# Performance work log

Measured on AMD Instinct MI355X. Metric: run time of the kernel, lower is better.

Reference implementation:

```python
import jax, jax.numpy as jnp
import numpy as np

B, LC, LM, D = 128, 512, 512, 512

def setup_inputs() -> dict:
    key = jax.random.key(0)
    k1, k2, k3 = jax.random.split(key, 3)
    context = jax.random.normal(k1, (B, LC, D), dtype=jnp.float32)
    main = jax.random.normal(k2, (B, LM, D), dtype=jnp.float32)
    W = jax.random.normal(k3, (D, 1), dtype=jnp.float32)
    return {"context": context, "main": main, "W": W}

def reference(context, main, W):
    # scores[b,c,m] = <context[b,c,:], main[b,m,:]>
    scores = jnp.einsum('bcd,bmd->bcm', context, main)
    # softmax over last axis (main positions), matching K.softmax default axis=-1
    attn = jax.nn.softmax(scores, axis=-1)           # [B, LC, LM]
    # Keras dot(axes=1): contract context-position axis -> [B, LM, D]
    aligned = jnp.einsum('bcm,bcd->bmd', attn, context)
    diff = main - aligned                            # [B, LM, D]
    # project to scalar per main position, softmax over positions
    w = jax.nn.softmax(jnp.einsum('bmd,d->bm', diff, W[:, 0]), axis=-1)  # [B, LM]
    # weighted sum over main positions -> [B, D]
    out = jnp.einsum('bm,bmd->bd', w, diff)
    return out
```

## Files before the change

### kernel.cpp

```cpp
#include <hip/hip_runtime.h>

#define B_  128
#define LC_ 512
#define LM_ 512
#define D_  512

typedef __attribute__((ext_vector_type(8))) short short8;
typedef __attribute__((ext_vector_type(16))) float f32x16;
typedef unsigned int u32;

__device__ __forceinline__ unsigned short bf16_rn(float x) {
  unsigned u = __float_as_uint(x);
  unsigned r = u + 0x7fffu + ((u >> 16) & 1u);
  return (unsigned short)(r >> 16);
}

__device__ __forceinline__ void gl_lds16(const void* g, void* l) {
  __builtin_amdgcn_global_load_lds((const __attribute__((address_space(1))) u32*)g,
                                   (__attribute__((address_space(3))) u32*)l, 16, 0, 0);
}

__global__ __launch_bounds__(256) void k_cvt_main(
    const float* __restrict__ mn, const float* __restrict__ W,
    short* __restrict__ BtH, short* __restrict__ BtL,
    float* __restrict__ v) {
  __shared__ float sW[512];
  int tid = threadIdx.x;
  sW[tid] = W[tid];
  sW[tid + 256] = W[tid + 256];
  __syncthreads();
  int wave = blockIdx.x * 4 + (tid >> 6);
  int b = wave >> 4, mt = wave & 15;
  int lane = tid & 63, rowl = lane & 31, h = lane >> 5;
  const float* src = mn + ((size_t)b * LM_ + 32 * mt + rowl) * D_ + 8 * h;
  float acc = 0.f;
  for (int ks = 0; ks < 32; ks++) {
    float4 f0 = *(const float4*)(src + 16 * ks);
    float4 f1 = *(const float4*)(src + 16 * ks + 4);
    float xs[8] = {f0.x, f0.y, f0.z, f0.w, f1.x, f1.y, f1.z, f1.w};
    int k = 16 * ks + 8 * h;
    float4 w0 = *(const float4*)&sW[k];
    float4 w1 = *(const float4*)&sW[k + 4];
    float ws[8] = {w0.x, w0.y, w0.z, w0.w, w1.x, w1.y, w1.z, w1.w};
    short8 vh, vl;
    #pragma unroll
    for (int e = 0; e < 8; e++) {
      unsigned short hb = bf16_rn(xs[e]);
      float hf = __uint_as_float((unsigned)hb << 16);
      vh[e] = (short)hb;
      vl[e] = (short)bf16_rn(xs[e] - hf);
      acc = fmaf(xs[e], ws[e], acc);
    }
    size_t off = (((size_t)b * 32 + ks) * 16 + mt) * 512 + (size_t)lane * 8;
    *(short8*)(BtH + off) = vh;
    *(short8*)(BtL + off) = vl;
  }
  acc += __shfl_xor(acc, 32, 64);
  if (h == 0) v[b * LM_ + 32 * mt + rowl] = acc;
}

struct __align__(16) Smem3 {
  short8 Bf[2][2][16][64];
  short8 Af[2][2][4][64];
  float sW[512];
  float red[4][128];
  float cmb[128];
  float uld[128];
  float tpw[2][4][128];
};

__global__ __launch_bounds__(512, 2) void k_scores_mfma3(
    const float* __restrict__ ctx, const short* __restrict__ BtH,
    const short* __restrict__ BtL, const float* __restrict__ W,
    float* __restrict__ P, float* __restrict__ tpart) {
  __shared__ Smem3 sm;
  int p = blockIdx.x;
  int b = (p & 7) | ((p >> 5) << 3);
  int cblk = (p >> 3) & 3;
  int c0 = cblk * 128;
  int tid = threadIdx.x;
  int lane = tid & 63, wv = tid >> 6;
  int rowl = lane & 31, h = lane >> 5;

  f32x16 acc[2][4];
  #pragma unroll
  for (int r = 0; r < 2; r++)
    #pragma unroll
    for (int mtl = 0; mtl < 4; mtl++)
      #pragma unroll
      for (int j = 0; j < 16; j++) acc[r][mtl][j] = 0.f;

  auto stageB = [&](int bf, int ks) {
    #pragma unroll
    for (int rep = 0; rep < 2; rep++) {
      int mt = wv + 8 * rep;
      size_t off = (((size_t)b * 32 + ks) * 16 + mt) * 512 + (size_t)lane * 8;
      gl_lds16(BtH + off, &sm.Bf[bf][0][mt][0]);
      gl_lds16(BtL + off, &sm.Bf[bf][1][mt][0]);
    }
  };
  auto cvtA = [&](int bf, int ks, const float4& g0, const float4& g1, float& au) {
    float xs[8] = {g0.x, g0.y, g0.z, g0.w, g1.x, g1.y, g1.z, g1.w};
    int k = 16 * ks + 8 * h;
    float4 w0 = *(const float4*)&sm.sW[k];
    float4 w1 = *(const float4*)&sm.sW[k + 4];
    float ws[8] = {w0.x, w0.y, w0.z, w0.w, w1.x, w1.y, w1.z, w1.w};
    short8 vh, vl;
    #pragma unroll
    for (int e = 0; e < 8; e++) {
      unsigned short hb = bf16_rn(xs[e]);
      float hf = __uint_as_float((unsigned)hb << 16);
      vh[e] = (short)hb;
      vl[e] = (short)bf16_rn(xs[e] - hf);
      au = fmaf(xs[e], ws[e], au);
    }
    *(short8*)&sm.Af[bf][0][wv][lane] = vh;
    *(short8*)&sm.Af[bf][1][wv][lane] = vl;
  };

  sm.sW[tid] = W[tid];
  float accu = 0.f;
  stageB(0, 0);
  const float* arow = ctx + ((size_t)b * LC_ + c0 + 32 * wv + rowl) * D_ + 8 * h;
  float4 g0, g1;
  if (wv < 4) {
    g0 = *(const float4*)(arow);
    g1 = *(const float4*)(arow + 4);
  }
  __syncthreads();
  if (wv < 4) cvtA(0, 0, g0, g1, accu);
  __syncthreads();

  for (int ks = 0; ks < 32; ks++) {
    int buf = ks & 1;
    if (ks < 31) {
      stageB(buf ^ 1, ks + 1);
      if (wv < 4) {
        const float* ap = arow + 16 * (ks + 1);
        g0 = *(const float4*)ap;
        g1 = *(const float4*)(ap + 4);
      }
    }
    int rt0 = (wv >> 2) * 2;
    short8 ah0 = sm.Af[buf][0][rt0][lane];
    short8 ah1 = sm.Af[buf][0][rt0 + 1][lane];
    short8 al0 = sm.Af[buf][1][rt0][lane];
    short8 al1 = sm.Af[buf][1][rt0 + 1][lane];
    #pragma unroll
    for (int mtl = 0; mtl < 4; mtl++) {
      int mtg = (wv & 3) * 4 + mtl;
      short8 bh = sm.Bf[buf][0][mtg][lane];
      short8 bl = sm.Bf[buf][1][mtg][lane];
      acc[0][mtl] = __builtin_amdgcn_mfma_f32_32x32x16_bf16(ah0, bh, acc[0][mtl], 0, 0, 0);
      acc[0][mtl] = __builtin_amdgcn_mfma_f32_32x32x16_bf16(ah0, bl, acc[0][mtl], 0, 0, 0);
      acc[0][mtl] = __builtin_amdgcn_mfma_f32_32x32x16_bf16(al0, bh, acc[0][mtl], 0, 0, 0);
      acc[1][mtl] = __builtin_amdgcn_mfma_f32_32x32x16_bf16(ah1, bh, acc[1][mtl], 0, 0, 0);
      acc[1][mtl] = __builtin_amdgcn_mfma_f32_32x32x16_bf16(ah1, bl, acc[1][mtl], 0, 0, 0);
      acc[1][mtl] = __builtin_amdgcn_mfma_f32_32x32x16_bf16(al1, bh, acc[1][mtl], 0, 0, 0);
    }
    if (ks < 31 && wv < 4) cvtA(buf ^ 1, ks + 1, g0, g1, accu);
    __syncthreads();
  }

  if (wv < 4) {
    accu += __shfl_xor(accu, 32, 64);
    if (h == 0) sm.uld[32 * wv + rowl] = accu;
  }

  #pragma unroll
  for (int r = 0; r < 2; r++)
    #pragma unroll
    for (int j = 0; j < 16; j++) {
      float mx = fmaxf(fmaxf(acc[r][0][j], acc[r][1][j]),
                       fmaxf(acc[r][2][j], acc[r][3][j]));
      #pragma unroll
      for (int s = 1; s <= 16; s <<= 1) mx = fmaxf(mx, __shfl_xor(mx, s, 64));
      if (rowl == 0)
        sm.red[wv & 3][64 * (wv >> 2) + 32 * r + (j & 3) + 8 * (j >> 2) + 4 * h] = mx;
    }
  __syncthreads();
  if (tid < 128)
    sm.cmb[tid] = fmaxf(fmaxf(sm.red[0][tid], sm.red[1][tid]),
                        fmaxf(sm.red[2][tid], sm.red[3][tid]));
  __syncthreads();
  #pragma unroll
  for (int r = 0; r < 2; r++)
    #pragma unroll
    for (int j = 0; j < 16; j++) {
      int row = 64 * (wv >> 2) + 32 * r + (j & 3) + 8 * (j >> 2) + 4 * h;
      float mx = sm.cmb[row];
      float s = 0.f;
      #pragma unroll
      for (int mtl = 0; mtl < 4; mtl++) {
        float e = __expf(acc[r][mtl][j] - mx);
        acc[r][mtl][j] = e;
        s += e;
      }
      #pragma unroll
      for (int st = 1; st <= 16; st <<= 1) s += __shfl_xor(s, st, 64);
      if (rowl == 0) sm.red[wv & 3][row] = s;
    }
  __syncthreads();
  if (tid < 128)
    sm.cmb[tid] = sm.red[0][tid] + sm.red[1][tid] + sm.red[2][tid] + sm.red[3][tid];
  __syncthreads();

  float* Pb = P + ((size_t)b * LC_ + c0) * LM_;
  float tp[4] = {0.f, 0.f, 0.f, 0.f};
  #pragma unroll
  for (int r = 0; r < 2; r++)
    #pragma unroll
    for (int j = 0; j < 16; j++) {
      int row = 64 * (wv >> 2) + 32 * r + (j & 3) + 8 * (j >> 2) + 4 * h;
      float rinv = 1.f / sm.cmb[row];
      float uu = sm.uld[row];
      #pragma unroll
      for (int mtl = 0; mtl < 4; mtl++) {
        float pv = acc[r][mtl][j] * rinv;
        Pb[(size_t)row * LM_ + 128 * (wv & 3) + 32 * mtl + rowl] = pv;
        tp[mtl] = fmaf(pv, uu, tp[mtl]);
      }
    }
  #pragma unroll
  for (int mtl = 0; mtl < 4; mtl++) tp[mtl] += __shfl_xor(tp[mtl], 32, 64);
  if (h == 0) {
    #pragma unroll
    for (int mtl = 0; mtl < 4; mtl++)
      sm.tpw[wv >> 2][wv & 3][32 * mtl + rowl] = tp[mtl];
  }
  __syncthreads();
  {
    int m = tid;
    tpart[((size_t)b * 4 + cblk) * LM_ + m] =
        sm.tpw[0][m >> 7][m & 127] + sm.tpw[1][m >> 7][m & 127];
  }
}

__global__ __launch_bounds__(256) void k_tw(const float* __restrict__ tpart,
                                            const float* __restrict__ v,
                                            float* __restrict__ w_) {
  int b = blockIdx.x;
  int tid = threadIdx.x;
  int m0 = tid * 2;
  const float* tp = tpart + (size_t)b * 4 * LM_;
  float s0 = 0.f, s1 = 0.f;
  #pragma unroll
  for (int cb = 0; cb < 4; cb++) {
    s0 += tp[cb * LM_ + m0];
    s1 += tp[cb * LM_ + m0 + 1];
  }
  float x0 = v[b * LM_ + m0] - s0;
  float x1 = v[b * LM_ + m0 + 1] - s1;
  float mx = fmaxf(x0, x1);
  #pragma unroll
  for (int s = 32; s >= 1; s >>= 1) mx = fmaxf(mx, __shfl_xor(mx, s, 64));
  __shared__ float redm[4], reds[4];
  int wvv = tid >> 6, ln = tid & 63;
  if (ln == 0) redm[wvv] = mx;
  __syncthreads();
  mx = fmaxf(fmaxf(redm[0], redm[1]), fmaxf(redm[2], redm[3]));
  float e0 = __expf(x0 - mx), e1 = __expf(x1 - mx);
  float sum = e0 + e1;
  #pragma unroll
  for (int s = 32; s >= 1; s >>= 1) sum += __shfl_xor(sum, s, 64);
  if (ln == 0) reds[wvv] = sum;
  __syncthreads();
  sum = reds[0] + reds[1] + reds[2] + reds[3];
  float rinv = 1.0f / sum;
  float2 o; o.x = e0 * rinv; o.y = e1 * rinv;
  *(float2*)&w_[b * LM_ + m0] = o;
}

__global__ __launch_bounds__(256) void k_q(const float* __restrict__ P,
                                           const float* __restrict__ w,
                                           float* __restrict__ q) {
  int b = blockIdx.y;
  int c0 = blockIdx.x * 32;
  int wvv = threadIdx.x >> 6, ln = threadIdx.x & 63;
  __shared__ float sw[LM_];
  *(float2*)&sw[threadIdx.x * 2] = *(const float2*)&w[b * LM_ + threadIdx.x * 2];
  __syncthreads();
  #pragma unroll
  for (int rr = 0; rr < 8; rr++) {
    int c = c0 + wvv * 8 + rr;
    const float4* Pr = (const float4*)(P + ((size_t)b * LC_ + c) * LM_) + ln * 2;
    float4 p0 = Pr[0], p1 = Pr[1];
    const float4* wr = (const float4*)sw + ln * 2;
    float4 w0 = wr[0], w1 = wr[1];
    float acc = p0.x*w0.x + p0.y*w0.y + p0.z*w0.z + p0.w*w0.w
              + p1.x*w1.x + p1.y*w1.y + p1.z*w1.z + p1.w*w1.w;
    #pragma unroll
    for (int s = 32; s >= 1; s >>= 1) acc += __shfl_xor(acc, s, 64);
    if (ln == 0) q[b * LC_ + c] = acc;
  }
}

__global__ __launch_bounds__(256) void k_out(const float* __restrict__ ctx,
                                             const float* __restrict__ mn,
                                             const float* __restrict__ w,
                                             const float* __restrict__ q,
                                             float* __restrict__ out) {
  int b = blockIdx.y;
  int d0 = blockIdx.x * 64;
  int td = threadIdx.x & 63;
  int tg = threadIdx.x >> 6;
  const float* Mb = mn  + (size_t)b * LM_ * D_ + d0;
  const float* Cb = ctx + (size_t)b * LC_ * D_ + d0;
  const float* wb = w + b * LM_;
  const float* qb = q + b * LC_;
  float acc = 0.f;
  #pragma unroll 4
  for (int m = tg; m < LM_; m += 4) acc += wb[m] * Mb[(size_t)m * D_ + td];
  #pragma unroll 4
  for (int c = tg; c < LC_; c += 4) acc -= qb[c] * Cb[(size_t)c * D_ + td];
  __shared__ float red[4][64];
  red[tg][td] = acc;
  __syncthreads();
  if (tg == 0)
    out[b * D_ + d0 + td] = red[0][td] + red[1][td] + red[2][td] + red[3][td];
}

extern "C" void kernel_launch(void* const* d_in, const int* in_sizes, int n_in,
                              void* d_out, int out_size, void* d_ws, size_t ws_size,
                              hipStream_t stream) {
  const float* ctx = (const float*)d_in[0];
  const float* mn  = (const float*)d_in[1];
  const float* W   = (const float*)d_in[2];
  float* out = (float*)d_out;

  char* base = (char*)d_ws;
  size_t nPbytes = (size_t)B_ * LC_ * LM_ * 4;
  size_t planeB  = (size_t)B_ * LM_ * D_ * 2;

  float* P   = (float*)base;
  short* BtH = (short*)(base + nPbytes);
  short* BtL = (short*)(base + nPbytes + planeB);
  char* p2 = base + nPbytes + 2 * planeB;
  float* tpart = (float*)p2;  p2 += (size_t)B_ * 4 * LM_ * 4;
  float* v = (float*)p2;      p2 += (size_t)B_ * LM_ * 4;
  float* w = (float*)p2;      p2 += (size_t)B_ * LM_ * 4;
  float* q = (float*)p2;

  k_cvt_main<<<dim3(512), 256, 0, stream>>>(mn, W, BtH, BtL, v);
  k_scores_mfma3<<<dim3(512), 512, 0, stream>>>(ctx, BtH, BtL, W, P, tpart);
  k_tw<<<dim3(B_), 256, 0, stream>>>(tpart, v, w);
  k_q<<<dim3(LC_ / 32, B_), 256, 0, stream>>>(P, w, q);
  k_out<<<dim3(D_ / 64, B_), 256, 0, stream>>>(ctx, mn, w, q, out);
}
```

Measured before the change: 281.8 us.

## Retile scores kernel to 64-row blocks with per-wave in-register A conversion

The scores kernel moves from 512-thread blocks covering 128 context rows to 256-thread blocks covering 64 rows, launched over twice as many blocks. Each wave now loads and splits its own context rows into bf16 hi/lo in registers, which removes the shared-memory A staging buffer and the extra barrier that went with it. Partial tp sums are written straight to an 8-way tpart array, and k_tw reduces over 8 slices instead of 4. The trade-off is that every wave redundantly converts the same A rows and global B staging doubles per output row, in exchange for less LDS use, fewer barriers and more blocks to spread across the device.

```diff
diff --git a/kernel.cpp b/kernel.cpp
--- a/kernel.cpp
+++ b/kernel.cpp
@@ -19,6 +19,13 @@
   __builtin_amdgcn_global_load_lds((const __attribute__((address_space(1))) u32*)g,
                                    (__attribute__((address_space(3))) u32*)l, 16, 0, 0);
 }
+
+#define CVT1(SRC, WS, AH, AL, IDX, ACCU)                         \
+  { unsigned short hb_ = bf16_rn(SRC);                           \
+    float hf_ = __uint_as_float((u32)hb_ << 16);                 \
+    AH[IDX] = (short)hb_;                                        \
+    AL[IDX] = (short)bf16_rn((SRC) - hf_);                       \
+    ACCU = fmaf((SRC), (WS), ACCU); }
 
 __global__ __launch_bounds__(256) void k_cvt_main(
     const float* __restrict__ mn, const float* __restrict__ W,
@@ -37,20 +44,14 @@
   for (int ks = 0; ks < 32; ks++) {
     float4 f0 = *(const float4*)(src + 16 * ks);
     float4 f1 = *(const float4*)(src + 16 * ks + 4);
-    float xs[8] = {f0.x, f0.y, f0.z, f0.w, f1.x, f1.y, f1.z, f1.w};
     int k = 16 * ks + 8 * h;
     float4 w0 = *(const float4*)&sW[k];
     float4 w1 = *(const float4*)&sW[k + 4];
-    float ws[8] = {w0.x, w0.y, w0.z, w0.w, w1.x, w1.y, w1.z, w1.w};
     short8 vh, vl;
-    #pragma unroll
-    for (int e = 0; e < 8; e++) {
-      unsigned short hb = bf16_rn(xs[e]);
-      float hf = __uint_as_float((unsigned)hb << 16);
-      vh[e] = (short)hb;
-      vl[e] = (short)bf16_rn(xs[e] - hf);
-      acc = fmaf(xs[e], ws[e], acc);
-    }
+    CVT1(f0.x, w0.x, vh, vl, 0, acc); CVT1(f0.y, w0.y, vh, vl, 1, acc);
+    CVT1(f0.z, w0.z, vh, vl, 2, acc); CVT1(f0.w, w0.w, vh, vl, 3, acc);
+    CVT1(f1.x, w1.x, vh, vl, 4, acc); CVT1(f1.y, w1.y, vh, vl, 5, acc);
+    CVT1(f1.z, w1.z, vh, vl, 6, acc); CVT1(f1.w, w1.w, vh, vl, 7, acc);
     size_t off = (((size_t)b * 32 + ks) * 16 + mt) * 512 + (size_t)lane * 8;
     *(short8*)(BtH + off) = vh;
     *(short8*)(BtL + off) = vl;
@@ -59,127 +60,117 @@
   if (h == 0) v[b * LM_ + 32 * mt + rowl] = acc;
 }
 
-struct __align__(16) Smem3 {
+struct __align__(16) Smem4 {
   short8 Bf[2][2][16][64];
-  short8 Af[2][2][4][64];
   float sW[512];
-  float red[4][128];
-  float cmb[128];
-  float uld[128];
-  float tpw[2][4][128];
+  float red[4][64];
+  float cmb[64];
+  float uld[64];
 };
 
-__global__ __launch_bounds__(512, 2) void k_scores_mfma3(
+__global__ __launch_bounds__(256, 2) void k_scores_mfma5(
     const float* __restrict__ ctx, const short* __restrict__ BtH,
     const short* __restrict__ BtL, const float* __restrict__ W,
     float* __restrict__ P, float* __restrict__ tpart) {
-  __shared__ Smem3 sm;
+  __shared__ Smem4 sm;
   int p = blockIdx.x;
-  int b = (p & 7) | ((p >> 5) << 3);
-  int cblk = (p >> 3) & 3;
-  int c0 = cblk * 128;
+  int b = (p & 7) | ((p >> 6) << 3);
+  int cblk = (p >> 3) & 7;
+  int c0 = cblk * 64;
   int tid = threadIdx.x;
   int lane = tid & 63, wv = tid >> 6;
   int rowl = lane & 31, h = lane >> 5;
 
-  f32x16 acc[2][4];
-  #pragma unroll
-  for (int r = 0; r < 2; r++)
-    #pragma unroll
-    for (int mtl = 0; mtl < 4; mtl++)
-      #pragma unroll
-      for (int j = 0; j < 16; j++) acc[r][mtl][j] = 0.f;
+  f32x16 acc0[4], acc1[4];
+  #pragma unroll
+  for (int m = 0; m < 4; m++)
+    #pragma unroll
+    for (int j = 0; j < 16; j++) { acc0[m][j] = 0.f; acc1[m][j] = 0.f; }
 
   auto stageB = [&](int bf, int ks) {
     #pragma unroll
-    for (int rep = 0; rep < 2; rep++) {
-      int mt = wv + 8 * rep;
+    for (int rep = 0; rep < 4; rep++) {
+      int mt = wv + 4 * rep;
       size_t off = (((size_t)b * 32 + ks) * 16 + mt) * 512 + (size_t)lane * 8;
       gl_lds16(BtH + off, &sm.Bf[bf][0][mt][0]);
       gl_lds16(BtL + off, &sm.Bf[bf][1][mt][0]);
     }
   };
-  auto cvtA = [&](int bf, int ks, const float4& g0, const float4& g1, float& au) {
-    float xs[8] = {g0.x, g0.y, g0.z, g0.w, g1.x, g1.y, g1.z, g1.w};
+
+  const float* ar0 = ctx + ((size_t)b * LC_ + c0 +      rowl) * D_ + 8 * h;
+  const float* ar1 = ctx + ((size_t)b * LC_ + c0 + 32 + rowl) * D_ + 8 * h;
+
+  sm.sW[tid] = W[tid];
+  sm.sW[tid + 256] = W[tid + 256];
+  stageB(0, 0);
+  float accu0 = 0.f, accu1 = 0.f;
+  __syncthreads();
+
+  for (int ks = 0; ks < 32; ks++) {
+    int buf = ks & 1;
+    if (ks < 31) stageB(buf ^ 1, ks + 1);
+
     int k = 16 * ks + 8 * h;
     float4 w0 = *(const float4*)&sm.sW[k];
     float4 w1 = *(const float4*)&sm.sW[k + 4];
-    float ws[8] = {w0.x, w0.y, w0.z, w0.w, w1.x, w1.y, w1.z, w1.w};
-    short8 vh, vl;
-    #pragma unroll
-    for (int e = 0; e < 8; e++) {
-      unsigned short hb = bf16_rn(xs[e]);
-      float hf = __uint_as_float((unsigned)hb << 16);
-      vh[e] = (short)hb;
-      vl[e] = (short)bf16_rn(xs[e] - hf);
-      au = fmaf(xs[e], ws[e], au);
-    }
-    *(short8*)&sm.Af[bf][0][wv][lane] = vh;
-    *(short8*)&sm.Af[bf][1][wv][lane] = vl;
-  };
-
-  sm.sW[tid] = W[tid];
-  float accu = 0.f;
-  stageB(0, 0);
-  const float* arow = ctx + ((size_t)b * LC_ + c0 + 32 * wv + rowl) * D_ + 8 * h;
-  float4 g0, g1;
-  if (wv < 4) {
-    g0 = *(const float4*)(arow);
-    g1 = *(const float4*)(arow + 4);
-  }
-  __syncthreads();
-  if (wv < 4) cvtA(0, 0, g0, g1, accu);
-  __syncthreads();
-
-  for (int ks = 0; ks < 32; ks++) {
-    int buf = ks & 1;
-    if (ks < 31) {
-      stageB(buf ^ 1, ks + 1);
-      if (wv < 4) {
-        const float* ap = arow + 16 * (ks + 1);
-        g0 = *(const float4*)ap;
-        g1 = *(const float4*)(ap + 4);
-      }
-    }
-    int rt0 = (wv >> 2) * 2;
-    short8 ah0 = sm.Af[buf][0][rt0][lane];
-    short8 ah1 = sm.Af[buf][0][rt0 + 1][lane];
-    short8 al0 = sm.Af[buf][1][rt0][lane];
-    short8 al1 = sm.Af[buf][1][rt0 + 1][lane];
+    short8 ah0, al0, ah1, al1;
+    {
+      const float* p0 = ar0 + 16 * ks;
+      float4 g0 = *(const float4*)p0;
+      float4 g1 = *(const float4*)(p0 + 4);
+      CVT1(g0.x, w0.x, ah0, al0, 0, accu0); CVT1(g0.y, w0.y, ah0, al0, 1, accu0);
+      CVT1(g0.z, w0.z, ah0, al0, 2, accu0); CVT1(g0.w, w0.w, ah0, al0, 3, accu0);
+      CVT1(g1.x, w1.x, ah0, al0, 4, accu0); CVT1(g1.y, w1.y, ah0, al0, 5, accu0);
+      CVT1(g1.z, w1.z, ah0, al0, 6, accu0); CVT1(g1.w, w1.w, ah0, al0, 7, accu0);
+    }
+    {
+      const float* p1 = ar1 + 16 * ks;
+      float4 g0 = *(const float4*)p1;
+      float4 g1 = *(const float4*)(p1 + 4);
+      CVT1(g0.x, w0.x, ah1, al1, 0, accu1); CVT1(g0.y, w0.y, ah1, al1, 1, accu1);
+      CVT1(g0.z, w0.z, ah1, al1, 2, accu1); CVT1(g0.w, w0.w, ah1, al1, 3, accu1);
+      CVT1(g1.x, w1.x, ah1, al1, 4, accu1); CVT1(g1.y, w1.y, ah1, al1, 5, accu1);
+      CVT1(g1.z, w1.z, ah1, al1, 6, accu1); CVT1(g1.w, w1.w, ah1, al1, 7, accu1);
+    }
+
     #pragma unroll
     for (int mtl = 0; mtl < 4; mtl++) {
-      int mtg = (wv & 3) * 4 + mtl;
-      short8 bh = sm.Bf[buf][0][mtg][lane];
-      short8 bl = sm.Bf[buf][1][mtg][lane];
-      acc[0][mtl] = __builtin_amdgcn_mfma_f32_32x32x16_bf16(ah0, bh, acc[0][mtl], 0, 0, 0);
-      acc[0][mtl] = __builtin_amdgcn_mfma_f32_32x32x16_bf16(ah0, bl, acc[0][mtl], 0, 0, 0);
-      acc[0][mtl] = __builtin_amdgcn_mfma_f32_32x32x16_bf16(al0, bh, acc[0][mtl], 0, 0, 0);
-      acc[1][mtl] = __builtin_amdgcn_mfma_f32_32x32x16_bf16(ah1, bh, acc[1][mtl], 0, 0, 0);
-      acc[1][mtl] = __builtin_amdgcn_mfma_f32_32x32x16_bf16(ah1, bl, acc[1][mtl], 0, 0, 0);
-      acc[1][mtl] = __builtin_amdgcn_mfma_f32_32x32x16_bf16(al1, bh, acc[1][mtl], 0, 0, 0);
-    }
-    if (ks < 31 && wv < 4) cvtA(buf ^ 1, ks + 1, g0, g1, accu);
+      int mt = 4 * wv + mtl;
+      short8 bh = sm.Bf[buf][0][mt][lane];
+      short8 bl = sm.Bf[buf][1][mt][lane];
+      acc0[mtl] = __builtin_amdgcn_mfma_f32_32x32x16_bf16(ah0, bh, acc0[mtl], 0, 0, 0);
+      acc0[mtl] = __builtin_amdgcn_mfma_f32_32x32x16_bf16(ah0, bl, acc0[mtl], 0, 0, 0);
+      acc0[mtl] = __builtin_amdgcn_mfma_f32_32x32x16_bf16(al0, bh, acc0[mtl], 0, 0, 0);
+      acc1[mtl] = __builtin_amdgcn_mfma_f32_32x32x16_bf16(ah1, bh, acc1[mtl], 0, 0, 0);
+      acc1[mtl] = __builtin_amdgcn_mfma_f32_32x32x16_bf16(ah1, bl, acc1[mtl], 0, 0, 0);
+      acc1[mtl] = __builtin_amdgcn_mfma_f32_32x32x16_bf16(al1, bh, acc1[mtl], 0, 0, 0);
+    }
     __syncthreads();
   }
 
-  if (wv < 4) {
-    accu += __shfl_xor(accu, 32, 64);
-    if (h == 0) sm.uld[32 * wv + rowl] = accu;
+  accu0 += __shfl_xor(accu0, 32, 64);
+  accu1 += __shfl_xor(accu1, 32, 64);
+  if (wv == 0 && h == 0) {
+    sm.uld[rowl] = accu0;
+    sm.uld[32 + rowl] = accu1;
   }
 
   #pragma unroll
   for (int r = 0; r < 2; r++)
     #pragma unroll
     for (int j = 0; j < 16; j++) {
-      float mx = fmaxf(fmaxf(acc[r][0][j], acc[r][1][j]),
-                       fmaxf(acc[r][2][j], acc[r][3][j]));
+      float a0 = r ? acc1[0][j] : acc0[0][j];
+      float a1 = r ? acc1[1][j] : acc0[1][j];
+      float a2 = r ? acc1[2][j] : acc0[2][j];
+      float a3 = r ? acc1[3][j] : acc0[3][j];
+      float mx = fmaxf(fmaxf(a0, a1), fmaxf(a2, a3));
       #pragma unroll
       for (int s = 1; s <= 16; s <<= 1) mx = fmaxf(mx, __shfl_xor(mx, s, 64));
       if (rowl == 0)
-        sm.red[wv & 3][64 * (wv >> 2) + 32 * r + (j & 3) + 8 * (j >> 2) + 4 * h] = mx;
-    }
-  __syncthreads();
-  if (tid < 128)
+        sm.red[wv][32 * r + (j & 3) + 8 * (j >> 2) + 4 * h] = mx;
+    }
+  __syncthreads();
+  if (tid < 64)
     sm.cmb[tid] = fmaxf(fmaxf(sm.red[0][tid], sm.red[1][tid]),
                         fmaxf(sm.red[2][tid], sm.red[3][tid]));
   __syncthreads();
@@ -187,21 +178,21 @@
   for (int r = 0; r < 2; r++)
     #pragma unroll
     for (int j = 0; j < 16; j++) {
-      int row = 64 * (wv >> 2) + 32 * r + (j & 3) + 8 * (j >> 2) + 4 * h;
+      int row = 32 * r + (j & 3) + 8 * (j >> 2) + 4 * h;
       float mx = sm.cmb[row];
       float s = 0.f;
       #pragma unroll
       for (int mtl = 0; mtl < 4; mtl++) {
-        float e = __expf(acc[r][mtl][j] - mx);
-        acc[r][mtl][j] = e;
+        float e = __expf((r ? acc1[mtl][j] : acc0[mtl][j]) - mx);
+        if (r) acc1[mtl][j] = e; else acc0[mtl][j] = e;
         s += e;
       }
       #pragma unroll
       for (int st = 1; st <= 16; st <<= 1) s += __shfl_xor(s, st, 64);
-      if (rowl == 0) sm.red[wv & 3][row] = s;
-    }
-  __syncthreads();
-  if (tid < 128)
+      if (rowl == 0) sm.red[wv][row] = s;
+    }
+  __syncthreads();
+  if (tid < 64)
     sm.cmb[tid] = sm.red[0][tid] + sm.red[1][tid] + sm.red[2][tid] + sm.red[3][tid];
   __syncthreads();
 
@@ -211,28 +202,23 @@
   for (int r = 0; r < 2; r++)
     #pragma unroll
     for (int j = 0; j < 16; j++) {
-      int row = 64 * (wv >> 2) + 32 * r + (j & 3) + 8 * (j >> 2) + 4 * h;
+      int row = 32 * r + (j & 3) + 8 * (j >> 2) + 4 * h;
       float rinv = 1.f / sm.cmb[row];
       float uu = sm.uld[row];
       #pragma unroll
       for (int mtl = 0; mtl < 4; mtl++) {
-        float pv = acc[r][mtl][j] * rinv;
-        Pb[(size_t)row * LM_ + 128 * (wv & 3) + 32 * mtl + rowl] = pv;
+        float pv = (r ? acc1[mtl][j] : acc0[mtl][j]) * rinv;
+        Pb[(size_t)row * LM_ + 128 * wv + 32 * mtl + rowl] = pv;
         tp[mtl] = fmaf(pv, uu, tp[mtl]);
       }
     }
   #pragma unroll
   for (int mtl = 0; mtl < 4; mtl++) tp[mtl] += __shfl_xor(tp[mtl], 32, 64);
   if (h == 0) {
+    float* tpb = tpart + ((size_t)b * 8 + cblk) * LM_;
     #pragma unroll
     for (int mtl = 0; mtl < 4; mtl++)
-      sm.tpw[wv >> 2][wv & 3][32 * mtl + rowl] = tp[mtl];
-  }
-  __syncthreads();
-  {
-    int m = tid;
-    tpart[((size_t)b * 4 + cblk) * LM_ + m] =
-        sm.tpw[0][m >> 7][m & 127] + sm.tpw[1][m >> 7][m & 127];
+      tpb[128 * wv + 32 * mtl + rowl] = tp[mtl];
   }
 }
 
@@ -242,10 +228,10 @@
   int b = blockIdx.x;
   int tid = threadIdx.x;
   int m0 = tid * 2;
-  const float* tp = tpart + (size_t)b * 4 * LM_;
+  const float* tp = tpart + (size_t)b * 8 * LM_;
   float s0 = 0.f, s1 = 0.f;
   #pragma unroll
-  for (int cb = 0; cb < 4; cb++) {
+  for (int cb = 0; cb < 8; cb++) {
     s0 += tp[cb * LM_ + m0];
     s1 += tp[cb * LM_ + m0 + 1];
   }
@@ -336,13 +322,13 @@
   short* BtH = (short*)(base + nPbytes);
   short* BtL = (short*)(base + nPbytes + planeB);
   char* p2 = base + nPbytes + 2 * planeB;
-  float* tpart = (float*)p2;  p2 += (size_t)B_ * 4 * LM_ * 4;
+  float* tpart = (float*)p2;  p2 += (size_t)B_ * 8 * LM_ * 4;
   float* v = (float*)p2;      p2 += (size_t)B_ * LM_ * 4;
   float* w = (float*)p2;      p2 += (size_t)B_ * LM_ * 4;
   float* q = (float*)p2;
 
   k_cvt_main<<<dim3(512), 256, 0, stream>>>(mn, W, BtH, BtL, v);
-  k_scores_mfma3<<<dim3(512), 512, 0, stream>>>(ctx, BtH, BtL, W, P, tpart);
+  k_scores_mfma5<<<dim3(1024), 256, 0, stream>>>(ctx, BtH, BtL, W, P, tpart);
   k_tw<<<dim3(B_), 256, 0, stream>>>(tpart, v, w);
   k_q<<<dim3(LC_ / 32, B_), 256, 0, stream>>>(P, w, q);
   k_out<<<dim3(D_ / 64, B_), 256, 0, stream>>>(ctx, mn, w, q, out);
```

New measurement: 344.8 us. 22.3% more time.

## Store attention probabilities as bf16 and read main from split-bf16 planes in k_out

Applied to the files above, without the earlier changes.

The softmax probability matrix P is now written as bf16 instead of fp32, halving its write and read traffic between the scores kernel and k_q. k_out reconstructs main from the already-computed hi/lo bf16 planes rather than the fp32 input, using the blocked layout. Rounding P to bf16 reduces accuracy of q and thus the output.

```diff
diff --git a/kernel.cpp b/kernel.cpp
--- a/kernel.cpp
+++ b/kernel.cpp
@@ -14,11 +14,20 @@
   unsigned r = u + 0x7fffu + ((u >> 16) & 1u);
   return (unsigned short)(r >> 16);
 }
-
+__device__ __forceinline__ float bf2f(short s) {
+  return __uint_as_float((u32)(unsigned short)s << 16);
+}
 __device__ __forceinline__ void gl_lds16(const void* g, void* l) {
   __builtin_amdgcn_global_load_lds((const __attribute__((address_space(1))) u32*)g,
                                    (__attribute__((address_space(3))) u32*)l, 16, 0, 0);
 }
+
+#define CVT1(SRC, WS, AH, AL, IDX, ACCU)                         \
+  { unsigned short hb_ = bf16_rn(SRC);                           \
+    float hf_ = __uint_as_float((u32)hb_ << 16);                 \
+    AH[IDX] = (short)hb_;                                        \
+    AL[IDX] = (short)bf16_rn((SRC) - hf_);                       \
+    ACCU = fmaf((SRC), (WS), ACCU); }
 
 __global__ __launch_bounds__(256) void k_cvt_main(
     const float* __restrict__ mn, const float* __restrict__ W,
@@ -37,20 +46,14 @@
   for (int ks = 0; ks < 32; ks++) {
     float4 f0 = *(const float4*)(src + 16 * ks);
     float4 f1 = *(const float4*)(src + 16 * ks + 4);
-    float xs[8] = {f0.x, f0.y, f0.z, f0.w, f1.x, f1.y, f1.z, f1.w};
     int k = 16 * ks + 8 * h;
     float4 w0 = *(const float4*)&sW[k];
     float4 w1 = *(const float4*)&sW[k + 4];
-    float ws[8] = {w0.x, w0.y, w0.z, w0.w, w1.x, w1.y, w1.z, w1.w};
     short8 vh, vl;
-    #pragma unroll
-    for (int e = 0; e < 8; e++) {
-      unsigned short hb = bf16_rn(xs[e]);
-      float hf = __uint_as_float((unsigned)hb << 16);
-      vh[e] = (short)hb;
-      vl[e] = (short)bf16_rn(xs[e] - hf);
-      acc = fmaf(xs[e], ws[e], acc);
-    }
+    CVT1(f0.x, w0.x, vh, vl, 0, acc); CVT1(f0.y, w0.y, vh, vl, 1, acc);
+    CVT1(f0.z, w0.z, vh, vl, 2, acc); CVT1(f0.w, w0.w, vh, vl, 3, acc);
+    CVT1(f1.x, w1.x, vh, vl, 4, acc); CVT1(f1.y, w1.y, vh, vl, 5, acc);
+    CVT1(f1.z, w1.z, vh, vl, 6, acc); CVT1(f1.w, w1.w, vh, vl, 7, acc);
     size_t off = (((size_t)b * 32 + ks) * 16 + mt) * 512 + (size_t)lane * 8;
     *(short8*)(BtH + off) = vh;
     *(short8*)(BtL + off) = vl;
@@ -69,10 +72,10 @@
   float tpw[2][4][128];
 };
 
-__global__ __launch_bounds__(512, 2) void k_scores_mfma3(
+__global__ __launch_bounds__(512, 2) void k_scores_mfma9(
     const float* __restrict__ ctx, const short* __restrict__ BtH,
     const short* __restrict__ BtL, const float* __restrict__ W,
-    float* __restrict__ P, float* __restrict__ tpart) {
+    unsigned short* __restrict__ P16, float* __restrict__ tpart) {
   __shared__ Smem3 sm;
   int p = blockIdx.x;
   int b = (p & 7) | ((p >> 5) << 3);
@@ -205,7 +208,7 @@
     sm.cmb[tid] = sm.red[0][tid] + sm.red[1][tid] + sm.red[2][tid] + sm.red[3][tid];
   __syncthreads();
 
-  float* Pb = P + ((size_t)b * LC_ + c0) * LM_;
+  unsigned short* Pb = P16 + ((size_t)b * LC_ + c0) * LM_;
   float tp[4] = {0.f, 0.f, 0.f, 0.f};
   #pragma unroll
   for (int r = 0; r < 2; r++)
@@ -217,7 +220,7 @@
       #pragma unroll
       for (int mtl = 0; mtl < 4; mtl++) {
         float pv = acc[r][mtl][j] * rinv;
-        Pb[(size_t)row * LM_ + 128 * (wv & 3) + 32 * mtl + rowl] = pv;
+        Pb[(size_t)row * LM_ + 128 * (wv & 3) + 32 * mtl + rowl] = bf16_rn(pv);
         tp[mtl] = fmaf(pv, uu, tp[mtl]);
       }
     }
@@ -271,7 +274,7 @@
   *(float2*)&w_[b * LM_ + m0] = o;
 }
 
-__global__ __launch_bounds__(256) void k_q(const float* __restrict__ P,
+__global__ __launch_bounds__(256) void k_q(const unsigned short* __restrict__ P16,
                                            const float* __restrict__ w,
                                            float* __restrict__ q) {
   int b = blockIdx.y;
@@ -283,12 +286,13 @@
   #pragma unroll
   for (int rr = 0; rr < 8; rr++) {
     int c = c0 + wvv * 8 + rr;
-    const float4* Pr = (const float4*)(P + ((size_t)b * LC_ + c) * LM_) + ln * 2;
-    float4 p0 = Pr[0], p1 = Pr[1];
-    const float4* wr = (const float4*)sw + ln * 2;
-    float4 w0 = wr[0], w1 = wr[1];
-    float acc = p0.x*w0.x + p0.y*w0.y + p0.z*w0.z + p0.w*w0.w
-              + p1.x*w1.x + p1.y*w1.y + p1.z*w1.z + p1.w*w1.w;
+    short8 pv = *((const short8*)(P16 + ((size_t)b * LC_ + c) * LM_) + ln);
+    float4 w0 = *(const float4*)&sw[ln * 8];
+    float4 w1 = *(const float4*)&sw[ln * 8 + 4];
+    float acc = bf2f(pv[0]) * w0.x + bf2f(pv[1]) * w0.y
+              + bf2f(pv[2]) * w0.z + bf2f(pv[3]) * w0.w
+              + bf2f(pv[4]) * w1.x + bf2f(pv[5]) * w1.y
+              + bf2f(pv[6]) * w1.z + bf2f(pv[7]) * w1.w;
     #pragma unroll
     for (int s = 32; s >= 1; s >>= 1) acc += __shfl_xor(acc, s, 64);
     if (ln == 0) q[b * LC_ + c] = acc;
@@ -296,28 +300,71 @@
 }
 
 __global__ __launch_bounds__(256) void k_out(const float* __restrict__ ctx,
-                                             const float* __restrict__ mn,
+                                             const short* __restrict__ BtH,
+                                             const short* __restrict__ BtL,
                                              const float* __restrict__ w,
                                              const float* __restrict__ q,
                                              float* __restrict__ out) {
   int b = blockIdx.y;
   int d0 = blockIdx.x * 64;
-  int td = threadIdx.x & 63;
-  int tg = threadIdx.x >> 6;
-  const float* Mb = mn  + (size_t)b * LM_ * D_ + d0;
+  int ks0 = d0 >> 4;
+  int tid = threadIdx.x;
+  int lane = tid & 63, wvv = tid >> 6;
+  int rowl = lane & 31, h = lane >> 5;
+  __shared__ float sw_[LM_];
+  __shared__ float redo[4][64];
+  __shared__ float red2[4][64];
+  sw_[tid] = w[b * LM_ + tid];
+  sw_[tid + 256] = w[b * LM_ + tid + 256];
+  __syncthreads();
+
+  float mp[4][8];
+  #pragma unroll
+  for (int ksl = 0; ksl < 4; ksl++)
+    #pragma unroll
+    for (int e = 0; e < 8; e++) mp[ksl][e] = 0.f;
+  for (int mt = wvv; mt < 16; mt += 4) {
+    float wm = sw_[32 * mt + rowl];
+    #pragma unroll
+    for (int ksl = 0; ksl < 4; ksl++) {
+      size_t off = (((size_t)b * 32 + ks0 + ksl) * 16 + mt) * 512 + (size_t)lane * 8;
+      short8 hh = *(const short8*)(BtH + off);
+      short8 ll = *(const short8*)(BtL + off);
+      #pragma unroll
+      for (int e = 0; e < 8; e++)
+        mp[ksl][e] = fmaf(wm, bf2f(hh[e]) + bf2f(ll[e]), mp[ksl][e]);
+    }
+  }
+  #pragma unroll
+  for (int ksl = 0; ksl < 4; ksl++)
+    #pragma unroll
+    for (int e = 0; e < 8; e++) {
+      float vsum = mp[ksl][e];
+      #pragma unroll
+      for (int s = 1; s <= 16; s <<= 1) vsum += __shfl_xor(vsum, s, 64);
+      mp[ksl][e] = vsum;
+    }
+  if (rowl == 0) {
+    #pragma unroll
+    for (int ksl = 0; ksl < 4; ksl++)
+      #pragma unroll
+      for (int e = 0; e < 8; e++)
+        redo[wvv][16 * ksl + 8 * h + e] = mp[ksl][e];
+  }
+
+  int td = tid & 63;
+  int tg = tid >> 6;
   const float* Cb = ctx + (size_t)b * LC_ * D_ + d0;
-  const float* wb = w + b * LM_;
   const float* qb = q + b * LC_;
   float acc = 0.f;
   #pragma unroll 4
-  for (int m = tg; m < LM_; m += 4) acc += wb[m] * Mb[(size_t)m * D_ + td];
-  #pragma unroll 4
   for (int c = tg; c < LC_; c += 4) acc -= qb[c] * Cb[(size_t)c * D_ + td];
-  __shared__ float red[4][64];
-  red[tg][td] = acc;
+  red2[tg][td] = acc;
   __syncthreads();
   if (tg == 0)
-    out[b * D_ + d0 + td] = red[0][td] + red[1][td] + red[2][td] + red[3][td];
+    out[b * D_ + d0 + td] =
+        redo[0][td] + redo[1][td] + redo[2][td] + redo[3][td] +
+        red2[0][td] + red2[1][td] + red2[2][td] + red2[3][td];
 }
 
 extern "C" void kernel_launch(void* const* d_in, const int* in_sizes, int n_in,
@@ -329,21 +376,21 @@
   float* out = (float*)d_out;
 
   char* base = (char*)d_ws;
-  size_t nPbytes = (size_t)B_ * LC_ * LM_ * 4;
-  size_t planeB  = (size_t)B_ * LM_ * D_ * 2;
-
-  float* P   = (float*)base;
-  short* BtH = (short*)(base + nPbytes);
-  short* BtL = (short*)(base + nPbytes + planeB);
-  char* p2 = base + nPbytes + 2 * planeB;
+  size_t nP16   = (size_t)B_ * LC_ * LM_ * 2;
+  size_t planeB = (size_t)B_ * LM_ * D_ * 2;
+
+  unsigned short* P16 = (unsigned short*)base;
+  short* BtH = (short*)(base + nP16);
+  short* BtL = (short*)(base + nP16 + planeB);
+  char* p2 = base + nP16 + 2 * planeB;
   float* tpart = (float*)p2;  p2 += (size_t)B_ * 4 * LM_ * 4;
   float* v = (float*)p2;      p2 += (size_t)B_ * LM_ * 4;
   float* w = (float*)p2;      p2 += (size_t)B_ * LM_ * 4;
   float* q = (float*)p2;
 
   k_cvt_main<<<dim3(512), 256, 0, stream>>>(mn, W, BtH, BtL, v);
-  k_scores_mfma3<<<dim3(512), 512, 0, stream>>>(ctx, BtH, BtL, W, P, tpart);
+  k_scores_mfma9<<<dim3(512), 512, 0, stream>>>(ctx, BtH, BtL, W, P16, tpart);
   k_tw<<<dim3(B_), 256, 0, stream>>>(tpart, v, w);
-  k_q<<<dim3(LC_ / 32, B_), 256, 0, stream>>>(P, w, q);
-  k_out<<<dim3(D_ / 64, B_), 256, 0, stream>>>(ctx, mn, w, q, out);
-}
+  k_q<<<dim3(LC_ / 32, B_), 256, 0, stream>>>(P16, w, q);
+  k_out<<<dim3(D_ / 64, B_), 256, 0, stream>>>(ctx, BtH, BtL, w, q, out);
+}
```

Result: faster. 255.5 us, median of 2 (-9.3%).
